# Kernel optimization log

Measured on AMD Instinct MI355X. Metric: run time of the kernel, lower is better.

The kernel has to match this reference:

```python
import jax, jax.numpy as jnp
import numpy as np

NUM_ROWS = 4096      # out_features
GROUP_COUNT = 32
GROUP_SIZE = 128     # in_features = GROUP_COUNT * GROUP_SIZE = 4096
CODEBOOK_SIZE = 16   # 4-bit codes


def setup_inputs() -> dict:
    key = jax.random.key(0)
    k1, k2, k3, k4 = jax.random.split(key, 4)
    x = jax.random.normal(k1, (2, 1024, GROUP_COUNT * GROUP_SIZE), dtype=jnp.float32)
    codebooks = jax.random.normal(k2, (NUM_ROWS, GROUP_COUNT, CODEBOOK_SIZE), dtype=jnp.float32)
    codes = jax.random.randint(k3, (NUM_ROWS, GROUP_COUNT, GROUP_SIZE), 0, CODEBOOK_SIZE, dtype=jnp.int32)
    bias = jax.random.normal(k4, (NUM_ROWS,), dtype=jnp.float32)
    return {"x": x, "codebooks": codebooks, "codes": codes, "bias": bias}


def _dequantize_weight(codes, codebooks):
    # codes: [R, G, S] int indices into last dim of codebooks [R, G, B]
    R, G, S = codes.shape
    W_hat = jnp.take_along_axis(codebooks, codes, axis=2)  # [R, G, S]
    return W_hat.reshape(R, G * S)  # [out_features, in_features]


def reference(x, codebooks, codes, bias):
    W = _dequantize_weight(codes, codebooks)           # [out, in]
    out = jnp.einsum("bsi,oi->bso", x, W) + bias       # F.linear
    return out
```

## Files before the change

### kernel.cpp

```cpp
#include <hip/hip_runtime.h>
#include <hip/hip_bf16.h>
#include <stdint.h>


#define M_DIM 2048
#define N_DIM 4096
#define K_DIM 4096

typedef __attribute__((ext_vector_type(4))) int i32x4;

__device__ __forceinline__ void async_load16(const void* g, void* l) {
    __builtin_amdgcn_global_load_lds(
        (const __attribute__((address_space(1))) uint32_t*)(uintptr_t)g,
        (__attribute__((address_space(3))) uint32_t*)(uint32_t)(uintptr_t)l,
        16, 0, 0);
}

__device__ __forceinline__ uint32_t pack4(int a, int b, int c, int d) {
    return (uint32_t)(a & 255) | ((uint32_t)(b & 255) << 8) |
           ((uint32_t)(c & 255) << 16) | ((uint32_t)(d & 255) << 24);
}

__device__ __forceinline__ int q8(float v, float inv) {
    return (int)rintf(v * inv);
}

__global__ __launch_bounds__(256) void prepass_q8(
    const float* __restrict__ cb,
    const int* __restrict__ codes,
    const float* __restrict__ x,
    uint32_t* __restrict__ wq,
    uint32_t* __restrict__ xq,
    float* __restrict__ sw,
    float* __restrict__ sx)
{
    __shared__ float scb[512];
    __shared__ float red[256];
    const int b = blockIdx.x, t = threadIdx.x;
    if (b < N_DIM) {
        const int o = b;
        const float c0 = cb[(size_t)o * 512 + t];
        const float c1 = cb[(size_t)o * 512 + 256 + t];
        scb[t] = c0; scb[t + 256] = c1;
        red[t] = fmaxf(fabsf(c0), fabsf(c1));
        __syncthreads();
        for (int s = 128; s > 0; s >>= 1) {
            if (t < s) red[t] = fmaxf(red[t], red[t + s]);
            __syncthreads();
        }
        const float amax = fmaxf(red[0], 1e-20f);
        const float inv = 127.0f / amax;
        if (t == 0) sw[o] = amax / 127.0f;
        const int* crow = codes + (size_t)o * K_DIM;
        uint32_t* orow = wq + (size_t)o * 1024;
#pragma unroll
        for (int i = 0; i < 4; ++i) {
            const int d = t + i * 256;
            const int4 c = *(const int4*)(crow + d * 4);
            const float* g = scb + (d >> 5) * 16;
            orow[d] = pack4(q8(g[c.x], inv), q8(g[c.y], inv),
                            q8(g[c.z], inv), q8(g[c.w], inv));
        }
    } else {
        const int m = b - N_DIM;
        const float* row = x + (size_t)m * K_DIM;
        float4 v[4];
        float am = 0.f;
#pragma unroll
        for (int i = 0; i < 4; ++i) {
            v[i] = *(const float4*)(row + (size_t)(t + i * 256) * 4);
            am = fmaxf(am, fmaxf(fmaxf(fabsf(v[i].x), fabsf(v[i].y)),
                                 fmaxf(fabsf(v[i].z), fabsf(v[i].w))));
        }
        red[t] = am;
        __syncthreads();
        for (int s = 128; s > 0; s >>= 1) {
            if (t < s) red[t] = fmaxf(red[t], red[t + s]);
            __syncthreads();
        }
        const float amax = fmaxf(red[0], 1e-20f);
        const float inv = 127.0f / amax;
        if (t == 0) sx[m] = amax / 127.0f;
        uint32_t* orow = xq + (size_t)m * 1024;
#pragma unroll
        for (int i = 0; i < 4; ++i)
            orow[t + i * 256] = pack4(q8(v[i].x, inv), q8(v[i].y, inv),
                                      q8(v[i].z, inv), q8(v[i].w, inv));
    }
}

__global__ __launch_bounds__(512, 4) void gemm_i8(
    const unsigned char* __restrict__ A,
    const unsigned char* __restrict__ B,
    const float* __restrict__ sx,
    const float* __restrict__ sw,
    const float* __restrict__ bias,
    float* __restrict__ C)
{
    __shared__ __align__(16) unsigned char smem[32768];
    unsigned char* As = smem;
    unsigned char* Bs = smem + 16384;

    const int tid  = threadIdx.x;
    const int w    = tid >> 6;
    const int lane = tid & 63;
    const int l15  = lane & 15;
    const int quad = lane >> 4;
    const int m0   = blockIdx.y * 128;
    const int n0   = blockIdx.x * 128;
    const int wk   = w >> 2;
    const int wm   = ((w >> 1) & 1) * 64;
    const int wn   = (w & 1) * 64;

    const int srow = tid >> 3;
    const int sc   = (tid & 7) ^ (srow & 7);
    const int scol = sc * 16;

    const unsigned char* gA0 = A + (size_t)(m0 +      srow) * K_DIM + scol;
    const unsigned char* gA1 = A + (size_t)(m0 + 64 + srow) * K_DIM + scol;
    const unsigned char* gB0 = B + (size_t)(n0 +      srow) * K_DIM + scol;
    const unsigned char* gB1 = B + (size_t)(n0 + 64 + srow) * K_DIM + scol;

    unsigned char* lA0 = As +        w * 1024;
    unsigned char* lA1 = As + 8192 + w * 1024;
    unsigned char* lB0 = Bs +        w * 1024;
    unsigned char* lB1 = Bs + 8192 + w * 1024;

    const int fs = (((wk << 2) + quad) ^ (l15 & 7)) * 16;

    i32x4 acc[4][4] = {};

    for (int k0 = 0; k0 < K_DIM; k0 += 128) {
        async_load16(gA0 + k0, lA0);
        async_load16(gA1 + k0, lA1);
        async_load16(gB0 + k0, lB0);
        async_load16(gB1 + k0, lB1);
        __syncthreads();

        i32x4 af[4], bfr[4];
#pragma unroll
        for (int i = 0; i < 4; ++i) {
            af[i]  = *(const i32x4*)(As + (wm + i * 16 + l15) * 128 + fs);
            bfr[i] = *(const i32x4*)(Bs + (wn + i * 16 + l15) * 128 + fs);
        }
#pragma unroll
        for (int mi = 0; mi < 4; ++mi)
#pragma unroll
            for (int ni = 0; ni < 4; ++ni)
                acc[mi][ni] = __builtin_amdgcn_mfma_i32_16x16x64_i8(
                    af[mi], bfr[ni], acc[mi][ni], 0, 0, 0);
        __syncthreads();
    }

    int* red = (int*)smem;
    if (w == 4 || w == 5) {
        int* dst = red + (w & 1) * 4096;
#pragma unroll
        for (int mi = 0; mi < 4; ++mi)
#pragma unroll
            for (int ni = 0; ni < 4; ++ni)
#pragma unroll
                for (int r = 0; r < 4; ++r)
                    dst[(((mi * 4 + ni) * 4) + r) * 64 + lane] = acc[mi][ni][r];
    }
    __syncthreads();
    if (w == 0 || w == 1) {
        const int* src = red + (w & 1) * 4096;
#pragma unroll
        for (int mi = 0; mi < 4; ++mi)
#pragma unroll
            for (int ni = 0; ni < 4; ++ni)
#pragma unroll
                for (int r = 0; r < 4; ++r)
                    acc[mi][ni][r] += src[(((mi * 4 + ni) * 4) + r) * 64 + lane];
    }
    __syncthreads();
    if (w == 6 || w == 7) {
        int* dst = red + (w & 1) * 4096;
#pragma unroll
        for (int mi = 0; mi < 4; ++mi)
#pragma unroll
            for (int ni = 0; ni < 4; ++ni)
#pragma unroll
                for (int r = 0; r < 4; ++r)
                    dst[(((mi * 4 + ni) * 4) + r) * 64 + lane] = acc[mi][ni][r];
    }
    __syncthreads();
    if (w == 2 || w == 3) {
        const int* src = red + (w & 1) * 4096;
#pragma unroll
        for (int mi = 0; mi < 4; ++mi)
#pragma unroll
            for (int ni = 0; ni < 4; ++ni)
#pragma unroll
                for (int r = 0; r < 4; ++r)
                    acc[mi][ni][r] += src[(((mi * 4 + ni) * 4) + r) * 64 + lane];
    }

    if (w < 4) {
        float sxv[4][4], swv[4], bv[4];
#pragma unroll
        for (int mi = 0; mi < 4; ++mi)
#pragma unroll
            for (int r = 0; r < 4; ++r)
                sxv[mi][r] = sx[m0 + wm + mi * 16 + quad * 4 + r];
#pragma unroll
        for (int ni = 0; ni < 4; ++ni) {
            const int col = n0 + wn + ni * 16 + l15;
            swv[ni] = sw[col];
            bv[ni]  = bias[col];
        }
#pragma unroll
        for (int mi = 0; mi < 4; ++mi) {
#pragma unroll
            for (int ni = 0; ni < 4; ++ni) {
                const int col = n0 + wn + ni * 16 + l15;
                float* cp = C + (size_t)(m0 + wm + mi * 16 + quad * 4) * N_DIM + col;
#pragma unroll
                for (int r = 0; r < 4; ++r)
                    cp[(size_t)r * N_DIM] =
                        (float)acc[mi][ni][r] * (sxv[mi][r] * swv[ni]) + bv[ni];
            }
        }
    }
}

__global__ __launch_bounds__(256) void naive_kernel(
    const float* __restrict__ x, const float* __restrict__ cb,
    const int* __restrict__ codes, const float* __restrict__ bias,
    float* __restrict__ out)
{
    const size_t idx = (size_t)blockIdx.x * 256 + threadIdx.x;
    const int n = (int)(idx & 4095);
    const int m = (int)(idx >> 12);
    const float* xr = x + (size_t)m * K_DIM;
    float s = bias[n];
    for (int g = 0; g < 32; ++g) {
        const float* cbr = cb + ((size_t)n * 32 + g) * 16;
        const int* cr = codes + ((size_t)n * 32 + g) * 128;
        const float* xg = xr + g * 128;
        for (int ss = 0; ss < 128; ++ss) s += xg[ss] * cbr[cr[ss]];
    }
    out[idx] = s;
}

extern "C" void kernel_launch(void* const* d_in, const int* in_sizes, int n_in,
                              void* d_out, int out_size, void* d_ws, size_t ws_size,
                              hipStream_t stream) {
    const float* x     = (const float*)d_in[0];
    const float* cb    = (const float*)d_in[1];
    const int*   codes = (const int*)d_in[2];
    const float* bias  = (const float*)d_in[3];
    float* out = (float*)d_out;

    const size_t szW = (size_t)N_DIM * K_DIM;
    const size_t szX = (size_t)M_DIM * K_DIM;
    const size_t need = szW + szX + (N_DIM + M_DIM) * sizeof(float);

    if (ws_size >= need) {
        unsigned char* Wq = (unsigned char*)d_ws;
        unsigned char* Xq = Wq + szW;
        float* sw = (float*)(Xq + szX);
        float* sx = sw + N_DIM;
        prepass_q8<<<dim3(N_DIM + M_DIM), dim3(256), 0, stream>>>(
            cb, codes, x, (uint32_t*)Wq, (uint32_t*)Xq, sw, sx);
        gemm_i8<<<dim3(N_DIM / 128, M_DIM / 128), dim3(512), 0, stream>>>(
            Xq, Wq, sx, sw, bias, out);
    } else {
        naive_kernel<<<dim3((M_DIM * N_DIM) / 256), dim3(256), 0, stream>>>(x, cb, codes, bias, out);
    }
}
```

Measured before the change: 172.1 us.

## Shrink GEMM tile to 64x128 with 256-thread blocks and simpler split-K reduction

Changes the int8 GEMM from 128x128 tiles with 8 waves (2-way split-K across 4 wave pairs) to 64x128 tiles with 4 waves (2-way split-K over 2 wave pairs). The grid becomes 1D with M-fastest ordering, so consecutive blocks share the same B (weight) tile. The cross-wave reduction now uses a single vectorized LDS exchange instead of two rounds. This doubles the block count for better CU occupancy and a shorter reduction tail, but halves A/B reuse per block, which raises global/L2 traffic.

New measurement: 185.8 us. 1.08x slower.

```diff
diff --git a/kernel.cpp b/kernel.cpp
--- a/kernel.cpp
+++ b/kernel.cpp
@@ -89,7 +89,7 @@
     }
 }
 
-__global__ __launch_bounds__(512, 4) void gemm_i8(
+__global__ __launch_bounds__(256, 4) void gemm_i8(
     const unsigned char* __restrict__ A,
     const unsigned char* __restrict__ B,
     const float* __restrict__ sx,
@@ -99,17 +99,17 @@
 {
     __shared__ __align__(16) unsigned char smem[32768];
     unsigned char* As = smem;
-    unsigned char* Bs = smem + 16384;
+    unsigned char* Bs = smem + 8192;
 
     const int tid  = threadIdx.x;
     const int w    = tid >> 6;
     const int lane = tid & 63;
     const int l15  = lane & 15;
     const int quad = lane >> 4;
-    const int m0   = blockIdx.y * 128;
-    const int n0   = blockIdx.x * 128;
-    const int wk   = w >> 2;
-    const int wm   = ((w >> 1) & 1) * 64;
+    const int bid  = blockIdx.x;
+    const int n0   = (bid >> 5) * 128;
+    const int m0   = (bid & 31) * 64;
+    const int wk   = w >> 1;
     const int wn   = (w & 1) * 64;
 
     const int srow = tid >> 3;
@@ -117,14 +117,18 @@
     const int scol = sc * 16;
 
     const unsigned char* gA0 = A + (size_t)(m0 +      srow) * K_DIM + scol;
-    const unsigned char* gA1 = A + (size_t)(m0 + 64 + srow) * K_DIM + scol;
+    const unsigned char* gA1 = A + (size_t)(m0 + 32 + srow) * K_DIM + scol;
     const unsigned char* gB0 = B + (size_t)(n0 +      srow) * K_DIM + scol;
-    const unsigned char* gB1 = B + (size_t)(n0 + 64 + srow) * K_DIM + scol;
+    const unsigned char* gB1 = B + (size_t)(n0 + 32 + srow) * K_DIM + scol;
+    const unsigned char* gB2 = B + (size_t)(n0 + 64 + srow) * K_DIM + scol;
+    const unsigned char* gB3 = B + (size_t)(n0 + 96 + srow) * K_DIM + scol;
 
     unsigned char* lA0 = As +        w * 1024;
-    unsigned char* lA1 = As + 8192 + w * 1024;
+    unsigned char* lA1 = As + 4096 + w * 1024;
     unsigned char* lB0 = Bs +        w * 1024;
-    unsigned char* lB1 = Bs + 8192 + w * 1024;
+    unsigned char* lB1 = Bs + 4096 + w * 1024;
+    unsigned char* lB2 = Bs + 8192 + w * 1024;
+    unsigned char* lB3 = Bs + 12288 + w * 1024;
 
     const int fs = (((wk << 2) + quad) ^ (l15 & 7)) * 16;
 
@@ -135,12 +139,14 @@
         async_load16(gA1 + k0, lA1);
         async_load16(gB0 + k0, lB0);
         async_load16(gB1 + k0, lB1);
+        async_load16(gB2 + k0, lB2);
+        async_load16(gB3 + k0, lB3);
         __syncthreads();
 
         i32x4 af[4], bfr[4];
 #pragma unroll
         for (int i = 0; i < 4; ++i) {
-            af[i]  = *(const i32x4*)(As + (wm + i * 16 + l15) * 128 + fs);
+            af[i]  = *(const i32x4*)(As + (     i * 16 + l15) * 128 + fs);
             bfr[i] = *(const i32x4*)(Bs + (wn + i * 16 + l15) * 128 + fs);
         }
 #pragma unroll
@@ -152,58 +158,34 @@
         __syncthreads();
     }
 
-    int* red = (int*)smem;
-    if (w == 4 || w == 5) {
-        int* dst = red + (w & 1) * 4096;
+    i32x4* red = (i32x4*)smem;
+    if (wk == 1) {
 #pragma unroll
         for (int mi = 0; mi < 4; ++mi)
 #pragma unroll
             for (int ni = 0; ni < 4; ++ni)
-#pragma unroll
-                for (int r = 0; r < 4; ++r)
-                    dst[(((mi * 4 + ni) * 4) + r) * 64 + lane] = acc[mi][ni][r];
+                red[(w & 1) * 1024 + (mi * 4 + ni) * 64 + lane] = acc[mi][ni];
     }
     __syncthreads();
-    if (w == 0 || w == 1) {
-        const int* src = red + (w & 1) * 4096;
-#pragma unroll
-        for (int mi = 0; mi < 4; ++mi)
-#pragma unroll
-            for (int ni = 0; ni < 4; ++ni)
-#pragma unroll
-                for (int r = 0; r < 4; ++r)
-                    acc[mi][ni][r] += src[(((mi * 4 + ni) * 4) + r) * 64 + lane];
-    }
-    __syncthreads();
-    if (w == 6 || w == 7) {
-        int* dst = red + (w & 1) * 4096;
-#pragma unroll
-        for (int mi = 0; mi < 4; ++mi)
-#pragma unroll
-            for (int ni = 0; ni < 4; ++ni)
-#pragma unroll
-                for (int r = 0; r < 4; ++r)
-                    dst[(((mi * 4 + ni) * 4) + r) * 64 + lane] = acc[mi][ni][r];
-    }
-    __syncthreads();
-    if (w == 2 || w == 3) {
-        const int* src = red + (w & 1) * 4096;
-#pragma unroll
-        for (int mi = 0; mi < 4; ++mi)
-#pragma unroll
-            for (int ni = 0; ni < 4; ++ni)
-#pragma unroll
-                for (int r = 0; r < 4; ++r)
-                    acc[mi][ni][r] += src[(((mi * 4 + ni) * 4) + r) * 64 + lane];
-    }
-
-    if (w < 4) {
+    if (wk == 0) {
+        const i32x4* src = red + (w & 1) * 1024;
+#pragma unroll
+        for (int mi = 0; mi < 4; ++mi)
+#pragma unroll
+            for (int ni = 0; ni < 4; ++ni) {
+                const i32x4 t = src[(mi * 4 + ni) * 64 + lane];
+#pragma unroll
+                for (int r = 0; r < 4; ++r) acc[mi][ni][r] += t[r];
+            }
+    }
+
+    if (wk == 0) {
         float sxv[4][4], swv[4], bv[4];
 #pragma unroll
         for (int mi = 0; mi < 4; ++mi)
 #pragma unroll
             for (int r = 0; r < 4; ++r)
-                sxv[mi][r] = sx[m0 + wm + mi * 16 + quad * 4 + r];
+                sxv[mi][r] = sx[m0 + mi * 16 + quad * 4 + r];
 #pragma unroll
         for (int ni = 0; ni < 4; ++ni) {
             const int col = n0 + wn + ni * 16 + l15;
@@ -215,7 +197,7 @@
 #pragma unroll
             for (int ni = 0; ni < 4; ++ni) {
                 const int col = n0 + wn + ni * 16 + l15;
-                float* cp = C + (size_t)(m0 + wm + mi * 16 + quad * 4) * N_DIM + col;
+                float* cp = C + (size_t)(m0 + mi * 16 + quad * 4) * N_DIM + col;
 #pragma unroll
                 for (int r = 0; r < 4; ++r)
                     cp[(size_t)r * N_DIM] =
@@ -264,7 +246,7 @@
         float* sx = sw + N_DIM;
         prepass_q8<<<dim3(N_DIM + M_DIM), dim3(256), 0, stream>>>(
             cb, codes, x, (uint32_t*)Wq, (uint32_t*)Xq, sw, sx);
-        gemm_i8<<<dim3(N_DIM / 128, M_DIM / 128), dim3(512), 0, stream>>>(
+        gemm_i8<<<dim3((N_DIM / 128) * (M_DIM / 64)), dim3(256), 0, stream>>>(
             Xq, Wq, sx, sw, bias, out);
     } else {
         naive_kernel<<<dim3((M_DIM * N_DIM) / 256), dim3(256), 0, stream>>>(x, cb, codes, bias, out);
```

## Double-buffer B tile in LDS and read A fragments directly from global

Applied to the files above, without the earlier changes.

The A operand no longer goes through LDS; each lane loads its MFMA fragments straight from global memory. The freed LDS holds a second B buffer, so the next B tile is prefetched asynchronously while the current one feeds the MFMAs, which removes one barrier per iteration. The cross-wave reduction now uses 16-byte vector LDS stores and loads. Global A loads are not coalesced across the K-split waves and have to come from cache, which risks higher latency on the critical path.

Result: slower. 209.9 us (+22.0%).

```diff
diff --git a/kernel.cpp b/kernel.cpp
--- a/kernel.cpp
+++ b/kernel.cpp
@@ -98,8 +98,8 @@
     float* __restrict__ C)
 {
     __shared__ __align__(16) unsigned char smem[32768];
-    unsigned char* As = smem;
-    unsigned char* Bs = smem + 16384;
+    unsigned char* Bs0 = smem;
+    unsigned char* Bs1 = smem + 16384;
 
     const int tid  = threadIdx.x;
     const int w    = tid >> 6;
@@ -114,90 +114,94 @@
 
     const int srow = tid >> 3;
     const int sc   = (tid & 7) ^ (srow & 7);
-    const int scol = sc * 16;
-
-    const unsigned char* gA0 = A + (size_t)(m0 +      srow) * K_DIM + scol;
-    const unsigned char* gA1 = A + (size_t)(m0 + 64 + srow) * K_DIM + scol;
-    const unsigned char* gB0 = B + (size_t)(n0 +      srow) * K_DIM + scol;
-    const unsigned char* gB1 = B + (size_t)(n0 + 64 + srow) * K_DIM + scol;
-
-    unsigned char* lA0 = As +        w * 1024;
-    unsigned char* lA1 = As + 8192 + w * 1024;
-    unsigned char* lB0 = Bs +        w * 1024;
-    unsigned char* lB1 = Bs + 8192 + w * 1024;
+    const unsigned char* gB0 = B + (size_t)(n0 +      srow) * K_DIM + sc * 16;
+    const unsigned char* gB1 = B + (size_t)(n0 + 64 + srow) * K_DIM + sc * 16;
+    const int lb0 = w * 1024;
+    const int lb1 = 8192 + w * 1024;
+
+    const unsigned char* gA = A + (size_t)(m0 + wm + l15) * K_DIM
+                                + ((wk << 2) + quad) * 16;
 
     const int fs = (((wk << 2) + quad) ^ (l15 & 7)) * 16;
 
     i32x4 acc[4][4] = {};
 
-    for (int k0 = 0; k0 < K_DIM; k0 += 128) {
-        async_load16(gA0 + k0, lA0);
-        async_load16(gA1 + k0, lA1);
-        async_load16(gB0 + k0, lB0);
-        async_load16(gB1 + k0, lB1);
-        __syncthreads();
+    async_load16(gB0, Bs0 + lb0);
+    async_load16(gB1, Bs0 + lb1);
+    __syncthreads();
+
+    for (int it = 0; it < 32; ++it) {
+        const int k0 = it * 128;
+        const unsigned char* cur = (it & 1) ? Bs1 : Bs0;
+        unsigned char*       nxt = (it & 1) ? Bs0 : Bs1;
+
+        if (it + 1 < 32) {
+            async_load16(gB0 + k0 + 128, nxt + lb0);
+            async_load16(gB1 + k0 + 128, nxt + lb1);
+        }
 
         i32x4 af[4], bfr[4];
 #pragma unroll
-        for (int i = 0; i < 4; ++i) {
-            af[i]  = *(const i32x4*)(As + (wm + i * 16 + l15) * 128 + fs);
-            bfr[i] = *(const i32x4*)(Bs + (wn + i * 16 + l15) * 128 + fs);
-        }
+        for (int i = 0; i < 4; ++i)
+            af[i] = *(const i32x4*)(gA + (size_t)i * 16 * K_DIM + k0);
+#pragma unroll
+        for (int i = 0; i < 4; ++i)
+            bfr[i] = *(const i32x4*)(cur + (wn + i * 16 + l15) * 128 + fs);
+
 #pragma unroll
         for (int mi = 0; mi < 4; ++mi)
 #pragma unroll
             for (int ni = 0; ni < 4; ++ni)
                 acc[mi][ni] = __builtin_amdgcn_mfma_i32_16x16x64_i8(
                     af[mi], bfr[ni], acc[mi][ni], 0, 0, 0);
+
         __syncthreads();
     }
 
-    int* red = (int*)smem;
+    i32x4* red = (i32x4*)smem;
     if (w == 4 || w == 5) {
-        int* dst = red + (w & 1) * 4096;
+        i32x4* dst = red + (w & 1) * 1024;
 #pragma unroll
         for (int mi = 0; mi < 4; ++mi)
 #pragma unroll
             for (int ni = 0; ni < 4; ++ni)
-#pragma unroll
-                for (int r = 0; r < 4; ++r)
-                    dst[(((mi * 4 + ni) * 4) + r) * 64 + lane] = acc[mi][ni][r];
+                dst[(mi * 4 + ni) * 64 + lane] = acc[mi][ni];
     }
     __syncthreads();
     if (w == 0 || w == 1) {
-        const int* src = red + (w & 1) * 4096;
+        const i32x4* src = red + (w & 1) * 1024;
+#pragma unroll
+        for (int mi = 0; mi < 4; ++mi)
+#pragma unroll
+            for (int ni = 0; ni < 4; ++ni) {
+                const i32x4 t = src[(mi * 4 + ni) * 64 + lane];
+#pragma unroll
+                for (int r = 0; r < 4; ++r) acc[mi][ni][r] += t[r];
+            }
+    }
+    __syncthreads();
+    if (w == 6 || w == 7) {
+        i32x4* dst = red + (w & 1) * 1024;
 #pragma unroll
         for (int mi = 0; mi < 4; ++mi)
 #pragma unroll
             for (int ni = 0; ni < 4; ++ni)
-#pragma unroll
-                for (int r = 0; r < 4; ++r)
-                    acc[mi][ni][r] += src[(((mi * 4 + ni) * 4) + r) * 64 + lane];
-    }
-    __syncthreads();
-    if (w == 6 || w == 7) {
-        int* dst = red + (w & 1) * 4096;
-#pragma unroll
-        for (int mi = 0; mi < 4; ++mi)
-#pragma unroll
-            for (int ni = 0; ni < 4; ++ni)
-#pragma unroll
-                for (int r = 0; r < 4; ++r)
-                    dst[(((mi * 4 + ni) * 4) + r) * 64 + lane] = acc[mi][ni][r];
+                dst[(mi * 4 + ni) * 64 + lane] = acc[mi][ni];
     }
     __syncthreads();
     if (w == 2 || w == 3) {
-        const int* src = red + (w & 1) * 4096;
-#pragma unroll
-        for (int mi = 0; mi < 4; ++mi)
-#pragma unroll
-            for (int ni = 0; ni < 4; ++ni)
-#pragma unroll
-                for (int r = 0; r < 4; ++r)
-                    acc[mi][ni][r] += src[(((mi * 4 + ni) * 4) + r) * 64 + lane];
-    }
-
-    if (w < 4) {
+        const i32x4* src = red + (w & 1) * 1024;
+#pragma unroll
+        for (int mi = 0; mi < 4; ++mi)
+#pragma unroll
+            for (int ni = 0; ni < 4; ++ni) {
+                const i32x4 t = src[(mi * 4 + ni) * 64 + lane];
+#pragma unroll
+                for (int r = 0; r < 4; ++r) acc[mi][ni][r] += t[r];
+            }
+    }
+
+    if (wk == 0) {
         float sxv[4][4], swv[4], bv[4];
 #pragma unroll
         for (int mi = 0; mi < 4; ++mi)
```
